# Kernel tuning notes

Measured on AMD Instinct MI355X. Metric: run time of the kernel, lower is better.

The kernel has to match this reference:

```python
import jax, jax.numpy as jnp
import numpy as np

N, E, K, G = 50000, 800000, 3, 64
F_IN, F_HID, F_OUT, N_CLS = 128, 192, 128, 10
LAMBDA_MAX = 2.0  # PyG ChebConv default when lambda_max is None and normalization='sym'


def setup_inputs() -> dict:
    key = jax.random.key(0)
    ks = jax.random.split(key, 12)
    x = jax.random.normal(ks[0], (N, F_IN), dtype=jnp.float32)
    edge_index = jax.random.randint(ks[1], (2, E), 0, N)
    batch = jnp.sort(jax.random.randint(ks[2], (N,), 0, G))

    def mkW(k, fi, fo):
        return jax.random.normal(k, (K, fi, fo), dtype=jnp.float32) / np.float32(np.sqrt(K * fi))

    W1 = mkW(ks[3], F_IN, F_HID)
    b1 = jax.random.normal(ks[4], (F_HID,), dtype=jnp.float32) * 0.01
    W2 = mkW(ks[5], F_HID, F_HID)
    b2 = jax.random.normal(ks[6], (F_HID,), dtype=jnp.float32) * 0.01
    W3 = mkW(ks[7], F_HID, F_OUT)
    b3 = jax.random.normal(ks[8], (F_OUT,), dtype=jnp.float32) * 0.01
    fc_w = jax.random.normal(ks[9], (F_OUT, N_CLS), dtype=jnp.float32) / np.float32(np.sqrt(F_OUT))
    fc_b = jax.random.normal(ks[10], (N_CLS,), dtype=jnp.float32) * 0.01
    return {"x": x, "edge_index": edge_index, "batch": batch,
            "W1": W1, "b1": b1, "W2": W2, "b2": b2, "W3": W3, "b3": b3,
            "fc_w": fc_w, "fc_b": fc_b}


def reference(x, edge_index, batch, W1, b1, W2, b2, W3, b3, fc_w, fc_b):
    row, col = edge_index[0], edge_index[1]
    # symmetric scaled Laplacian: L_hat = (2/lmax) * (I - D^-1/2 A D^-1/2) - I
    deg = jax.ops.segment_sum(jnp.ones((E,), x.dtype), row, num_segments=N)
    dis = jnp.where(deg > 0, jax.lax.rsqrt(jnp.maximum(deg, 1e-12)), 0.0)
    scale = 2.0 / LAMBDA_MAX
    w_edge = (-scale) * dis[row] * dis[col]  # off-diagonal entries of L_hat
    diag_w = scale - 1.0                      # diagonal entries (0 when lmax=2)

    def prop(h):  # h: [N, F] -> L_hat @ h
        return jax.ops.segment_sum(w_edge[:, None] * h[col], row, num_segments=N) + diag_w * h

    def cheb_conv(h, W, b):
        Tx0 = h
        out = Tx0 @ W[0]
        Tx1 = prop(Tx0)
        out = out + Tx1 @ W[1]
        for k in range(2, K):
            Tx2 = 2.0 * prop(Tx1) - Tx0
            out = out + Tx2 @ W[k]
            Tx0, Tx1 = Tx1, Tx2
        return out + b

    h = cheb_conv(x, W1, b1)
    h = cheb_conv(h, W2, b2)
    h = cheb_conv(h, W3, b3)

    # global mean pool over graphs
    sums = jax.ops.segment_sum(h, batch, num_segments=G)
    cnts = jax.ops.segment_sum(jnp.ones((N,), h.dtype), batch, num_segments=G)
    pooled = sums / jnp.maximum(cnts, 1.0)[:, None]  # [G, F_OUT]

    logits = pooled @ fc_w + fc_b
    return jax.nn.log_softmax(logits, axis=1)
```

## Files before the change

### kernel.cpp

```cpp
#include <hip/hip_runtime.h>
#include <math.h>

#define N_NODES 50000
#define N_EDGES 800000
#define N_GRAPHS 64
#define F_INN 128
#define F_HID 192
#define F_OUTT 128
#define N_CLS 10

typedef short short8 __attribute__((ext_vector_type(8)));
typedef float f32x4 __attribute__((ext_vector_type(4)));

static __device__ inline unsigned short f2bf(float f) {
    unsigned int u = __float_as_uint(f);
    unsigned int r = (u + 0x7FFFu + ((u >> 16) & 1u)) >> 16;
    return (unsigned short)r;
}
static __device__ inline float bf2f(unsigned short h) {
    return __uint_as_float(((unsigned int)h) << 16);
}

__global__ void k_deg(const int* __restrict__ row, int* __restrict__ cnt,
                      int* __restrict__ rank) {
    int e = blockIdx.x * 256 + threadIdx.x;
    if (e < N_EDGES) rank[e] = atomicAdd(&cnt[row[e]], 1);
}

__global__ void k_scan1(const int* __restrict__ cnt, int* __restrict__ rp,
                        int* __restrict__ part, float* __restrict__ dis) {
    __shared__ int s[256];
    int base = blockIdx.x * 512;
    int i0 = base + 2 * threadIdx.x;
    int v0 = (i0 < N_NODES) ? cnt[i0] : 0;
    int v1 = (i0 + 1 < N_NODES) ? cnt[i0 + 1] : 0;
    if (i0 < N_NODES) dis[i0] = v0 > 0 ? rsqrtf((float)v0) : 0.f;
    if (i0 + 1 < N_NODES) dis[i0 + 1] = v1 > 0 ? rsqrtf((float)v1) : 0.f;
    int tsum = v0 + v1;
    s[threadIdx.x] = tsum;
    __syncthreads();
    for (int off = 1; off < 256; off <<= 1) {
        int val = (threadIdx.x >= off) ? s[threadIdx.x - off] : 0;
        __syncthreads();
        s[threadIdx.x] += val;
        __syncthreads();
    }
    int excl = s[threadIdx.x] - tsum;
    if (i0 < N_NODES) rp[i0] = excl;
    if (i0 + 1 < N_NODES) rp[i0 + 1] = excl + v0;
    if (threadIdx.x == 255) part[blockIdx.x] = s[255];
}

__global__ void k_scan3(int* __restrict__ rp, const int* __restrict__ part,
                        int nb) {
    __shared__ int s[128];
    int t = threadIdx.x;
    int b = blockIdx.x;
    if (t < 128) s[t] = (t < b && t < nb) ? part[t] : 0;
    __syncthreads();
    for (int off = 64; off > 0; off >>= 1) {
        if (t < off) s[t] += s[t + off];
        __syncthreads();
    }
    int add = s[0];
    int i0 = b * 512 + 2 * t;
    if (i0 < N_NODES) rp[i0] += add;
    if (i0 + 1 < N_NODES) rp[i0 + 1] += add;
    if (b == 0 && t == 0) rp[N_NODES] = N_EDGES;
}

__global__ void k_scatter(const int* __restrict__ row, const int* __restrict__ col,
                          const float* __restrict__ dis, const int* __restrict__ rp,
                          const int* __restrict__ rank, int2* __restrict__ cw) {
    int e = blockIdx.x * 256 + threadIdx.x;
    if (e < N_EDGES) {
        int r = row[e], c = col[e];
        int pos = rp[r] + rank[e];
        int2 v;
        v.x = c;
        v.y = __float_as_int(-dis[r] * dis[c]);
        cw[pos] = v;
    }
}

#define NX (N_NODES * F_INN)
#define NW1 (3 * 128 * 192)
#define NW2 (3 * 192 * 192)
#define NW3 (3 * 192 * 128)
#define NPS (N_GRAPHS * F_OUTT)
__global__ void k_convAll(const float* __restrict__ x, const float* __restrict__ W1,
                          const float* __restrict__ W2, const float* __restrict__ W3,
                          unsigned short* __restrict__ xb,
                          unsigned short* __restrict__ Wt1,
                          unsigned short* __restrict__ Wt2,
                          unsigned short* __restrict__ Wt3,
                          int* __restrict__ cnt, float* __restrict__ psum) {
    int idx = blockIdx.x * 256 + threadIdx.x;
    if (idx < NX) {
        xb[idx] = f2bf(x[idx]);
        return;
    }
    idx -= NX;
    if (idx < NW1) {
        int per = 128 * 192;
        int j = idx / per, r = idx - j * per;
        int k = r / 192, n = r - k * 192;
        float v = (j == 0) ? (W1[idx] - W1[idx + 2 * per])
                           : (j == 2 ? 2.f * W1[idx] : W1[idx]);
        Wt1[j * per + n * 128 + k] = f2bf(v);
        return;
    }
    idx -= NW1;
    if (idx < NW2) {
        int per = 192 * 192;
        int j = idx / per, r = idx - j * per;
        int k = r / 192, n = r - k * 192;
        float v = (j == 0) ? (W2[idx] - W2[idx + 2 * per])
                           : (j == 2 ? 2.f * W2[idx] : W2[idx]);
        Wt2[j * per + n * 192 + k] = f2bf(v);
        return;
    }
    idx -= NW2;
    if (idx < NW3) {
        int per = 192 * 128;
        int j = idx / per, r = idx - j * per;
        int k = r / 128, n = r - k * 128;
        float v = (j == 0) ? (W3[idx] - W3[idx + 2 * per])
                           : (j == 2 ? 2.f * W3[idx] : W3[idx]);
        Wt3[j * per + n * 192 + k] = f2bf(v);
        return;
    }
    idx -= NW3;
    if (idx < N_NODES) {
        cnt[idx] = 0;
        return;
    }
    idx -= N_NODES;
    if (idx < NPS) psum[idx] = 0.f;
}

template <int F>
__global__ void k_spmv(const int* __restrict__ rp, const int2* __restrict__ cw,
                       const unsigned short* __restrict__ h,
                       unsigned short* __restrict__ y) {
    constexpr bool EX = (F > 128);
    constexpr int FU = F / 2;
    int wave = threadIdx.x >> 6;
    int lane = threadIdx.x & 63;
    int r = blockIdx.x * 4 + wave;
    if (r >= N_NODES) return;
    int e0 = __builtin_amdgcn_readfirstlane(rp[r]);
    int e1 = __builtin_amdgcn_readfirstlane(rp[r + 1]);
    const unsigned int* hu = (const unsigned int*)h;
    float a0 = 0.f, a1 = 0.f, a2 = 0.f;
    int e = e0;
    for (; e + 8 <= e1; e += 8) {
        int colv[8];
        float wv[8];
#pragma unroll
        for (int u = 0; u < 8; u++) {
            int2 p = cw[e + u];
            colv[u] = __builtin_amdgcn_readfirstlane(p.x);
            wv[u] = __uint_as_float(__builtin_amdgcn_readfirstlane(p.y));
        }
        unsigned int g[8];
        unsigned short s[8];
#pragma unroll
        for (int u = 0; u < 8; u++) {
            g[u] = hu[colv[u] * FU + lane];
            if constexpr (EX) s[u] = h[colv[u] * F + 128 + lane];
        }
#pragma unroll
        for (int u = 0; u < 8; u++) {
            a0 += wv[u] * bf2f((unsigned short)g[u]);
            a1 += wv[u] * bf2f((unsigned short)(g[u] >> 16));
            if constexpr (EX) a2 += wv[u] * bf2f(s[u]);
        }
    }
    for (; e + 4 <= e1; e += 4) {
        int colv[4];
        float wv[4];
#pragma unroll
        for (int u = 0; u < 4; u++) {
            int2 p = cw[e + u];
            colv[u] = __builtin_amdgcn_readfirstlane(p.x);
            wv[u] = __uint_as_float(__builtin_amdgcn_readfirstlane(p.y));
        }
        unsigned int g[4];
        unsigned short s[4];
#pragma unroll
        for (int u = 0; u < 4; u++) {
            g[u] = hu[colv[u] * FU + lane];
            if constexpr (EX) s[u] = h[colv[u] * F + 128 + lane];
        }
#pragma unroll
        for (int u = 0; u < 4; u++) {
            a0 += wv[u] * bf2f((unsigned short)g[u]);
            a1 += wv[u] * bf2f((unsigned short)(g[u] >> 16));
            if constexpr (EX) a2 += wv[u] * bf2f(s[u]);
        }
    }
    for (; e < e1; e++) {
        int2 p = cw[e];
        int c = __builtin_amdgcn_readfirstlane(p.x);
        float w = __uint_as_float(__builtin_amdgcn_readfirstlane(p.y));
        unsigned int g = hu[c * FU + lane];
        a0 += w * bf2f((unsigned short)g);
        a1 += w * bf2f((unsigned short)(g >> 16));
        if constexpr (EX) a2 += w * bf2f(h[c * F + 128 + lane]);
    }
    ((unsigned int*)y)[r * FU + lane] =
        (unsigned int)f2bf(a0) | ((unsigned int)f2bf(a1) << 16);
    if constexpr (EX) y[r * F + 128 + lane] = f2bf(a2);
}

template <int Fin, int Fout, bool FUSE_POOL>
__global__ __launch_bounds__(256) void k_gemm3(
    const unsigned short* __restrict__ A0, const unsigned short* __restrict__ A1,
    const unsigned short* __restrict__ A2, const unsigned short* __restrict__ Wt,
    const float* __restrict__ bias, unsigned short* __restrict__ C,
    const int* __restrict__ batch, float* __restrict__ psum) {
    constexpr int NF = Fout / 16;
    constexpr int BP = Fout / 64;
    __shared__ unsigned short As[128 * 40];
    __shared__ unsigned short Bs[Fout * 40];
    int t = threadIdx.x;
    int w = t >> 6;
    int lane = t & 63;
    int ml = lane & 15;
    int quad = lane >> 4;
    int mBase = blockIdx.x * 128;
    constexpr int per = Fin * Fout;

    f32x4 acc[2][NF];
#pragma unroll
    for (int i = 0; i < 2; i++)
#pragma unroll
        for (int jn = 0; jn < NF; jn++) acc[i][jn] = (f32x4){0.f, 0.f, 0.f, 0.f};

    int srow = t >> 2;
    int schunk = t & 3;
    constexpr int nChunks = (3 * Fin) >> 5;

    for (int ch = 0; ch < nChunks; ch++) {
        int kg = ch << 5;
        int j = kg / Fin;
        int kk = kg - j * Fin;
        const unsigned short* Aj = (j == 0) ? A0 : (j == 1) ? A1 : A2;
        if (ch > 0) __syncthreads();
#pragma unroll
        for (int pass = 0; pass < 2; pass++) {
            int row = srow + pass * 64;
            int gm = mBase + row;
            uint4 v = {0u, 0u, 0u, 0u};
            if (gm < N_NODES)
                v = *(const uint4*)(Aj + (size_t)gm * Fin + kk + schunk * 8);
            *(uint4*)&As[row * 40 + schunk * 8] = v;
        }
#pragma unroll
        for (int pass = 0; pass < BP; pass++) {
            int row = srow + pass * 64;
            const unsigned short* src =
                Wt + (size_t)j * per + (size_t)row * Fin + kk + schunk * 8;
            *(uint4*)&Bs[row * 40 + schunk * 8] = *(const uint4*)src;
        }
        __syncthreads();

        short8 afr[2];
#pragma unroll
        for (int i = 0; i < 2; i++)
            afr[i] = *(const short8*)&As[(w * 32 + i * 16 + ml) * 40 + quad * 8];
#pragma unroll
        for (int jn = 0; jn < NF; jn++) {
            short8 bfr = *(const short8*)&Bs[(jn * 16 + ml) * 40 + quad * 8];
#pragma unroll
            for (int i = 0; i < 2; i++)
                acc[i][jn] = __builtin_amdgcn_mfma_f32_16x16x32_bf16(
                    afr[i], bfr, acc[i][jn], 0, 0, 0);
        }
    }

    float biasv[NF];
#pragma unroll
    for (int jn = 0; jn < NF; jn++) biasv[jn] = bias[jn * 16 + ml];

    if constexpr (!FUSE_POOL) {
#pragma unroll
        for (int i = 0; i < 2; i++) {
#pragma unroll
            for (int r = 0; r < 4; r++) {
                int m = mBase + w * 32 + i * 16 + quad * 4 + r;
                if (m < N_NODES) {
                    unsigned short* cp = C + (size_t)m * Fout + ml;
#pragma unroll
                    for (int jn = 0; jn < NF; jn++)
                        cp[jn * 16] = f2bf(acc[i][jn][r] + biasv[jn]);
                }
            }
        }
    } else {
        int m0 = mBase + w * 32;
        if (m0 >= N_NODES) return;
        int mlast = m0 + 31;
        if (mlast >= N_NODES) mlast = N_NODES - 1;
        int g0 = batch[m0];
        int g1 = batch[mlast];
        if (g0 == g1) {
#pragma unroll
            for (int jn = 0; jn < NF; jn++) {
                float pv = 0.f;
#pragma unroll
                for (int i = 0; i < 2; i++)
#pragma unroll
                    for (int r = 0; r < 4; r++) {
                        int m = m0 + i * 16 + quad * 4 + r;
                        if (m < N_NODES) pv += acc[i][jn][r] + biasv[jn];
                    }
                pv += __shfl_xor(pv, 16);
                pv += __shfl_xor(pv, 32);
                if (lane < 16) atomicAdd(&psum[g0 * F_OUTT + ml + jn * 16], pv);
            }
        } else {
#pragma unroll
            for (int i = 0; i < 2; i++)
#pragma unroll
                for (int r = 0; r < 4; r++) {
                    int m = m0 + i * 16 + quad * 4 + r;
                    if (m < N_NODES) {
                        int g = batch[m];
#pragma unroll
                        for (int jn = 0; jn < NF; jn++)
                            atomicAdd(&psum[g * F_OUTT + ml + jn * 16],
                                      acc[i][jn][r] + biasv[jn]);
                    }
                }
        }
    }
}

__global__ void k_head(const float* __restrict__ psum, const int* __restrict__ batch,
                       const float* __restrict__ fcw, const float* __restrict__ fcb,
                       float* __restrict__ out) {
    int g = blockIdx.x;
    int c = threadIdx.x;
    __shared__ float sl[N_CLS];
    int a = 0, b = N_NODES;
    while (a < b) { int m = (a + b) >> 1; if (batch[m] < g) a = m + 1; else b = m; }
    int lo = a;
    a = lo; b = N_NODES;
    while (a < b) { int m = (a + b) >> 1; if (batch[m] < g + 1) a = m + 1; else b = m; }
    float inv = 1.f / fmaxf((float)(a - lo), 1.f);
    float l = 0.f;
    if (c < N_CLS) {
        l = fcb[c];
        for (int k = 0; k < F_OUTT; k++)
            l += psum[g * F_OUTT + k] * inv * fcw[k * N_CLS + c];
        sl[c] = l;
    }
    __syncthreads();
    if (c < N_CLS) {
        float m = -1e30f;
        for (int i = 0; i < N_CLS; i++) m = fmaxf(m, sl[i]);
        float s = 0.f;
        for (int i = 0; i < N_CLS; i++) s += expf(sl[i] - m);
        out[g * N_CLS + c] = l - m - logf(s);
    }
}

extern "C" void kernel_launch(void* const* d_in, const int* in_sizes, int n_in,
                              void* d_out, int out_size, void* d_ws, size_t ws_size,
                              hipStream_t stream) {
    const float* x = (const float*)d_in[0];
    const int* ei = (const int*)d_in[1];
    const int* batch = (const int*)d_in[2];
    const float* W1 = (const float*)d_in[3];
    const float* b1 = (const float*)d_in[4];
    const float* W2 = (const float*)d_in[5];
    const float* b2 = (const float*)d_in[6];
    const float* W3 = (const float*)d_in[7];
    const float* b3 = (const float*)d_in[8];
    const float* fcw = (const float*)d_in[9];
    const float* fcb = (const float*)d_in[10];
    float* out = (float*)d_out;
    const int* row = ei;
    const int* col = ei + N_EDGES;

    char* p = (char*)d_ws;
    auto carve = [&](size_t bytes) {
        char* q = p;
        p += (bytes + 255) & ~(size_t)255;
        return q;
    };
    int* cnt = (int*)carve(N_NODES * 4);
    int* rank = (int*)carve((size_t)N_EDGES * 4);
    float* dis = (float*)carve(N_NODES * 4);
    int* rp = (int*)carve((N_NODES + 1) * 4);
    int* part = (int*)carve(128 * 4);
    int2* cw = (int2*)carve((size_t)N_EDGES * 8);
    unsigned short* xb = (unsigned short*)carve((size_t)N_NODES * F_INN * 2);
    size_t hbytes = (size_t)N_NODES * 192 * 2;
    unsigned short* bufA = (unsigned short*)carve(hbytes);
    unsigned short* bufB = (unsigned short*)carve(hbytes);
    unsigned short* bufC = (unsigned short*)carve(hbytes);
    unsigned short* bufD = (unsigned short*)carve(hbytes);
    unsigned short* Wt1 = (unsigned short*)carve(NW1 * 2);
    unsigned short* Wt2 = (unsigned short*)carve(NW2 * 2);
    unsigned short* Wt3 = (unsigned short*)carve(NW3 * 2);
    float* psum = (float*)carve(NPS * 4);

    {
        int tot = NX + NW1 + NW2 + NW3 + N_NODES + NPS;
        k_convAll<<<(tot + 255) / 256, 256, 0, stream>>>(x, W1, W2, W3, xb, Wt1, Wt2,
                                                         Wt3, cnt, psum);
    }

    k_deg<<<(N_EDGES + 255) / 256, 256, 0, stream>>>(row, cnt, rank);
    int nb = (N_NODES + 511) / 512;
    k_scan1<<<nb, 256, 0, stream>>>(cnt, rp, part, dis);
    k_scan3<<<nb, 256, 0, stream>>>(rp, part, nb);
    k_scatter<<<(N_EDGES + 255) / 256, 256, 0, stream>>>(row, col, dis, rp, rank, cw);

    const int spmvGrid = (N_NODES + 3) / 4;
    const int gemmGrid = (N_NODES + 127) / 128;

    k_spmv<128><<<spmvGrid, 256, 0, stream>>>(rp, cw, xb, bufB);
    k_spmv<128><<<spmvGrid, 256, 0, stream>>>(rp, cw, bufB, bufC);
    k_gemm3<128, 192, false><<<gemmGrid, 256, 0, stream>>>(xb, bufB, bufC, Wt1, b1,
                                                           bufA, batch, psum);
    k_spmv<192><<<spmvGrid, 256, 0, stream>>>(rp, cw, bufA, bufB);
    k_spmv<192><<<spmvGrid, 256, 0, stream>>>(rp, cw, bufB, bufC);
    k_gemm3<192, 192, false><<<gemmGrid, 256, 0, stream>>>(bufA, bufB, bufC, Wt2, b2,
                                                           bufD, batch, psum);
    k_spmv<192><<<spmvGrid, 256, 0, stream>>>(rp, cw, bufD, bufB);
    k_spmv<192><<<spmvGrid, 256, 0, stream>>>(rp, cw, bufB, bufC);
    k_gemm3<192, 128, true><<<gemmGrid, 256, 0, stream>>>(bufD, bufB, bufC, Wt3, b3,
                                                          nullptr, batch, psum);

    k_head<<<N_GRAPHS, 64, 0, stream>>>(psum, batch, fcw, fcb, out);
}
```

Baseline: 456.3 us.

## Pool before final Chebyshev GEMM and compress edge list to 16-bit columns

Uses linearity of mean pooling to drop the third layer's big GEMM. Pooled sums of h, L·h and L²·h are accumulated into psum, and the 192→128 projection is done per graph in the head kernel. The edge array shrinks from (int col, float weight) pairs to 16-bit column indices, and the weight is recomputed in the SpMV from dis values, which cuts edge-stream bandwidth. Risks are atomic contention on psum in the last two SpMVs, extra gathers of dis[col], and the 16-bit index only holding while N fits in 65536.

```diff
diff --git a/kernel.cpp b/kernel.cpp
--- a/kernel.cpp
+++ b/kernel.cpp
@@ -19,6 +19,9 @@
 }
 static __device__ inline float bf2f(unsigned short h) {
     return __uint_as_float(((unsigned int)h) << 16);
+}
+static __device__ inline float rfl_f(float v) {
+    return __uint_as_float(__builtin_amdgcn_readfirstlane(__float_as_uint(v)));
 }
 
 __global__ void k_deg(const int* __restrict__ row, int* __restrict__ cnt,
@@ -70,16 +73,12 @@
 }
 
 __global__ void k_scatter(const int* __restrict__ row, const int* __restrict__ col,
-                          const float* __restrict__ dis, const int* __restrict__ rp,
-                          const int* __restrict__ rank, int2* __restrict__ cw) {
+                          const int* __restrict__ rp, const int* __restrict__ rank,
+                          unsigned short* __restrict__ cols16) {
     int e = blockIdx.x * 256 + threadIdx.x;
     if (e < N_EDGES) {
-        int r = row[e], c = col[e];
-        int pos = rp[r] + rank[e];
-        int2 v;
-        v.x = c;
-        v.y = __float_as_int(-dis[r] * dis[c]);
-        cw[pos] = v;
+        int r = row[e];
+        cols16[rp[r] + rank[e]] = (unsigned short)col[e];
     }
 }
 
@@ -87,7 +86,7 @@
 #define NW1 (3 * 128 * 192)
 #define NW2 (3 * 192 * 192)
 #define NW3 (3 * 192 * 128)
-#define NPS (N_GRAPHS * F_OUTT)
+#define NPS (3 * N_GRAPHS * F_HID)
 __global__ void k_convAll(const float* __restrict__ x, const float* __restrict__ W1,
                           const float* __restrict__ W2, const float* __restrict__ W3,
                           unsigned short* __restrict__ xb,
@@ -139,82 +138,109 @@
     if (idx < NPS) psum[idx] = 0.f;
 }
 
-template <int F>
-__global__ void k_spmv(const int* __restrict__ rp, const int2* __restrict__ cw,
+template <int F, int POOL>
+__global__ void k_spmv(const int* __restrict__ rp,
+                       const unsigned short* __restrict__ cols,
+                       const float* __restrict__ dis,
                        const unsigned short* __restrict__ h,
-                       unsigned short* __restrict__ y) {
+                       unsigned short* __restrict__ y,
+                       const int* __restrict__ batch, float* __restrict__ psum) {
     constexpr bool EX = (F > 128);
     constexpr int FU = F / 2;
+    __shared__ float ps[POOL ? 192 : 1];
+    __shared__ int gs[4];
     int wave = threadIdx.x >> 6;
     int lane = threadIdx.x & 63;
     int r = blockIdx.x * 4 + wave;
-    if (r >= N_NODES) return;
     int e0 = __builtin_amdgcn_readfirstlane(rp[r]);
     int e1 = __builtin_amdgcn_readfirstlane(rp[r + 1]);
+    float ndisr = -rfl_f(dis[r]);
     const unsigned int* hu = (const unsigned int*)h;
     float a0 = 0.f, a1 = 0.f, a2 = 0.f;
     int e = e0;
     for (; e + 8 <= e1; e += 8) {
         int colv[8];
-        float wv[8];
-#pragma unroll
-        for (int u = 0; u < 8; u++) {
-            int2 p = cw[e + u];
-            colv[u] = __builtin_amdgcn_readfirstlane(p.x);
-            wv[u] = __uint_as_float(__builtin_amdgcn_readfirstlane(p.y));
-        }
+#pragma unroll
+        for (int u = 0; u < 8; u++)
+            colv[u] = __builtin_amdgcn_readfirstlane((int)cols[e + u]);
         unsigned int g[8];
         unsigned short s[8];
+        float dv[8];
 #pragma unroll
         for (int u = 0; u < 8; u++) {
             g[u] = hu[colv[u] * FU + lane];
             if constexpr (EX) s[u] = h[colv[u] * F + 128 + lane];
+            dv[u] = rfl_f(dis[colv[u]]);
         }
 #pragma unroll
         for (int u = 0; u < 8; u++) {
-            a0 += wv[u] * bf2f((unsigned short)g[u]);
-            a1 += wv[u] * bf2f((unsigned short)(g[u] >> 16));
-            if constexpr (EX) a2 += wv[u] * bf2f(s[u]);
+            float w = ndisr * dv[u];
+            a0 += w * bf2f((unsigned short)g[u]);
+            a1 += w * bf2f((unsigned short)(g[u] >> 16));
+            if constexpr (EX) a2 += w * bf2f(s[u]);
         }
     }
     for (; e + 4 <= e1; e += 4) {
         int colv[4];
-        float wv[4];
-#pragma unroll
-        for (int u = 0; u < 4; u++) {
-            int2 p = cw[e + u];
-            colv[u] = __builtin_amdgcn_readfirstlane(p.x);
-            wv[u] = __uint_as_float(__builtin_amdgcn_readfirstlane(p.y));
-        }
+#pragma unroll
+        for (int u = 0; u < 4; u++)
+            colv[u] = __builtin_amdgcn_readfirstlane((int)cols[e + u]);
         unsigned int g[4];
         unsigned short s[4];
+        float dv[4];
 #pragma unroll
         for (int u = 0; u < 4; u++) {
             g[u] = hu[colv[u] * FU + lane];
             if constexpr (EX) s[u] = h[colv[u] * F + 128 + lane];
+            dv[u] = rfl_f(dis[colv[u]]);
         }
 #pragma unroll
         for (int u = 0; u < 4; u++) {
-            a0 += wv[u] * bf2f((unsigned short)g[u]);
-            a1 += wv[u] * bf2f((unsigned short)(g[u] >> 16));
-            if constexpr (EX) a2 += wv[u] * bf2f(s[u]);
+            float w = ndisr * dv[u];
+            a0 += w * bf2f((unsigned short)g[u]);
+            a1 += w * bf2f((unsigned short)(g[u] >> 16));
+            if constexpr (EX) a2 += w * bf2f(s[u]);
         }
     }
     for (; e < e1; e++) {
-        int2 p = cw[e];
-        int c = __builtin_amdgcn_readfirstlane(p.x);
-        float w = __uint_as_float(__builtin_amdgcn_readfirstlane(p.y));
+        int c = __builtin_amdgcn_readfirstlane((int)cols[e]);
+        float w = ndisr * rfl_f(dis[c]);
         unsigned int g = hu[c * FU + lane];
         a0 += w * bf2f((unsigned short)g);
         a1 += w * bf2f((unsigned short)(g >> 16));
         if constexpr (EX) a2 += w * bf2f(h[c * F + 128 + lane]);
     }
-    ((unsigned int*)y)[r * FU + lane] =
-        (unsigned int)f2bf(a0) | ((unsigned int)f2bf(a1) << 16);
-    if constexpr (EX) y[r * F + 128 + lane] = f2bf(a2);
-}
-
-template <int Fin, int Fout, bool FUSE_POOL>
+    if constexpr (POOL != 1) {
+        ((unsigned int*)y)[r * FU + lane] =
+            (unsigned int)f2bf(a0) | ((unsigned int)f2bf(a1) << 16);
+        if constexpr (EX) y[r * F + 128 + lane] = f2bf(a2);
+    }
+    if constexpr (POOL != 0) {
+        int t = threadIdx.x;
+        if (t < 4) gs[t] = batch[blockIdx.x * 4 + t];
+        if (t >= 64) ps[t - 64] = 0.f;
+        __syncthreads();
+        int g0 = gs[0], g3 = gs[3];
+        if (g0 == g3) {
+            atomicAdd(&ps[2 * lane], a0);
+            atomicAdd(&ps[2 * lane + 1], a1);
+            atomicAdd(&ps[128 + lane], a2);
+            __syncthreads();
+            if (wave == 0) {
+                atomicAdd(&psum[g0 * 192 + 2 * lane], ps[2 * lane]);
+                atomicAdd(&psum[g0 * 192 + 2 * lane + 1], ps[2 * lane + 1]);
+                atomicAdd(&psum[g0 * 192 + 128 + lane], ps[128 + lane]);
+            }
+        } else {
+            int gg = gs[wave];
+            atomicAdd(&psum[gg * 192 + 2 * lane], a0);
+            atomicAdd(&psum[gg * 192 + 2 * lane + 1], a1);
+            atomicAdd(&psum[gg * 192 + 128 + lane], a2);
+        }
+    }
+}
+
+template <int Fin, int Fout, bool POOL>
 __global__ __launch_bounds__(256) void k_gemm3(
     const unsigned short* __restrict__ A0, const unsigned short* __restrict__ A1,
     const unsigned short* __restrict__ A2, const unsigned short* __restrict__ Wt,
@@ -284,21 +310,20 @@
 #pragma unroll
     for (int jn = 0; jn < NF; jn++) biasv[jn] = bias[jn * 16 + ml];
 
-    if constexpr (!FUSE_POOL) {
-#pragma unroll
-        for (int i = 0; i < 2; i++) {
-#pragma unroll
-            for (int r = 0; r < 4; r++) {
-                int m = mBase + w * 32 + i * 16 + quad * 4 + r;
-                if (m < N_NODES) {
-                    unsigned short* cp = C + (size_t)m * Fout + ml;
-#pragma unroll
-                    for (int jn = 0; jn < NF; jn++)
-                        cp[jn * 16] = f2bf(acc[i][jn][r] + biasv[jn]);
-                }
+#pragma unroll
+    for (int i = 0; i < 2; i++) {
+#pragma unroll
+        for (int r = 0; r < 4; r++) {
+            int m = mBase + w * 32 + i * 16 + quad * 4 + r;
+            if (m < N_NODES) {
+                unsigned short* cp = C + (size_t)m * Fout + ml;
+#pragma unroll
+                for (int jn = 0; jn < NF; jn++)
+                    cp[jn * 16] = f2bf(acc[i][jn][r] + biasv[jn]);
             }
         }
-    } else {
+    }
+    if constexpr (POOL) {
         int m0 = mBase + w * 32;
         if (m0 >= N_NODES) return;
         int mlast = m0 + 31;
@@ -318,7 +343,7 @@
                     }
                 pv += __shfl_xor(pv, 16);
                 pv += __shfl_xor(pv, 32);
-                if (lane < 16) atomicAdd(&psum[g0 * F_OUTT + ml + jn * 16], pv);
+                if (lane < 16) atomicAdd(&psum[g0 * Fout + ml + jn * 16], pv);
             }
         } else {
 #pragma unroll
@@ -330,7 +355,7 @@
                         int g = batch[m];
 #pragma unroll
                         for (int jn = 0; jn < NF; jn++)
-                            atomicAdd(&psum[g * F_OUTT + ml + jn * 16],
+                            atomicAdd(&psum[g * Fout + ml + jn * 16],
                                       acc[i][jn][r] + biasv[jn]);
                     }
                 }
@@ -338,32 +363,56 @@
     }
 }
 
-__global__ void k_head(const float* __restrict__ psum, const int* __restrict__ batch,
-                       const float* __restrict__ fcw, const float* __restrict__ fcb,
-                       float* __restrict__ out) {
+__global__ __launch_bounds__(128) void k_head2(
+    const float* __restrict__ psum,
+    const unsigned short* __restrict__ Wt3, const float* __restrict__ b3,
+    const int* __restrict__ batch, const float* __restrict__ fcw,
+    const float* __restrict__ fcb, float* __restrict__ out) {
     int g = blockIdx.x;
-    int c = threadIdx.x;
+    int t = threadIdx.x;
+    __shared__ float ps[3 * 192];
+    __shared__ float m3[F_OUTT];
     __shared__ float sl[N_CLS];
+    for (int i = t; i < 192; i += 128) {
+        ps[i] = psum[g * 192 + i];
+        ps[192 + i] = psum[N_GRAPHS * 192 + g * 192 + i];
+        ps[384 + i] = psum[2 * N_GRAPHS * 192 + g * 192 + i];
+    }
+    __syncthreads();
     int a = 0, b = N_NODES;
     while (a < b) { int m = (a + b) >> 1; if (batch[m] < g) a = m + 1; else b = m; }
     int lo = a;
     a = lo; b = N_NODES;
     while (a < b) { int m = (a + b) >> 1; if (batch[m] < g + 1) a = m + 1; else b = m; }
     float inv = 1.f / fmaxf((float)(a - lo), 1.f);
-    float l = 0.f;
-    if (c < N_CLS) {
-        l = fcb[c];
-        for (int k = 0; k < F_OUTT; k++)
-            l += psum[g * F_OUTT + k] * inv * fcw[k * N_CLS + c];
-        sl[c] = l;
-    }
+    constexpr int per = 192 * F_OUTT;
+    float accv = 0.f;
+    const unsigned short* wp = Wt3 + (size_t)t * 192;
+#pragma unroll 4
+    for (int k = 0; k < 192; k += 8) {
+        short8 v0 = *(const short8*)(wp + k);
+        short8 v1 = *(const short8*)(wp + per + k);
+        short8 v2 = *(const short8*)(wp + 2 * per + k);
+#pragma unroll
+        for (int j = 0; j < 8; j++)
+            accv += ps[k + j] * bf2f((unsigned short)v0[j]) +
+                    ps[192 + k + j] * bf2f((unsigned short)v1[j]) +
+                    ps[384 + k + j] * bf2f((unsigned short)v2[j]);
+    }
+    m3[t] = accv * inv + b3[t];
     __syncthreads();
-    if (c < N_CLS) {
-        float m = -1e30f;
-        for (int i = 0; i < N_CLS; i++) m = fmaxf(m, sl[i]);
+    if (t < N_CLS) {
+        float l = fcb[t];
+        for (int n = 0; n < F_OUTT; n++) l += m3[n] * fcw[n * N_CLS + t];
+        sl[t] = l;
+    }
+    __syncthreads();
+    if (t < N_CLS) {
+        float mx = -1e30f;
+        for (int i = 0; i < N_CLS; i++) mx = fmaxf(mx, sl[i]);
         float s = 0.f;
-        for (int i = 0; i < N_CLS; i++) s += expf(sl[i] - m);
-        out[g * N_CLS + c] = l - m - logf(s);
+        for (int i = 0; i < N_CLS; i++) s += expf(sl[i] - mx);
+        out[g * N_CLS + t] = sl[t] - mx - logf(s);
     }
 }
 
@@ -396,7 +445,7 @@
     float* dis = (float*)carve(N_NODES * 4);
     int* rp = (int*)carve((N_NODES + 1) * 4);
     int* part = (int*)carve(128 * 4);
-    int2* cw = (int2*)carve((size_t)N_EDGES * 8);
+    unsigned short* cols16 = (unsigned short*)carve((size_t)N_EDGES * 2);
     unsigned short* xb = (unsigned short*)carve((size_t)N_NODES * F_INN * 2);
     size_t hbytes = (size_t)N_NODES * 192 * 2;
     unsigned short* bufA = (unsigned short*)carve(hbytes);
@@ -407,6 +456,9 @@
     unsigned short* Wt2 = (unsigned short*)carve(NW2 * 2);
     unsigned short* Wt3 = (unsigned short*)carve(NW3 * 2);
     float* psum = (float*)carve(NPS * 4);
+    float* psumX = psum;
+    float* psumG1 = psum + N_GRAPHS * 192;
+    float* psumG2 = psum + 2 * N_GRAPHS * 192;
 
     {
         int tot = NX + NW1 + NW2 + NW3 + N_NODES + NPS;
@@ -418,23 +470,27 @@
     int nb = (N_NODES + 511) / 512;
     k_scan1<<<nb, 256, 0, stream>>>(cnt, rp, part, dis);
     k_scan3<<<nb, 256, 0, stream>>>(rp, part, nb);
-    k_scatter<<<(N_EDGES + 255) / 256, 256, 0, stream>>>(row, col, dis, rp, rank, cw);
-
-    const int spmvGrid = (N_NODES + 3) / 4;
+    k_scatter<<<(N_EDGES + 255) / 256, 256, 0, stream>>>(row, col, rp, rank, cols16);
+
+    const int spmvGrid = N_NODES / 4;
     const int gemmGrid = (N_NODES + 127) / 128;
 
-    k_spmv<128><<<spmvGrid, 256, 0, stream>>>(rp, cw, xb, bufB);
-    k_spmv<128><<<spmvGrid, 256, 0, stream>>>(rp, cw, bufB, bufC);
+    k_spmv<128, 0><<<spmvGrid, 256, 0, stream>>>(rp, cols16, dis, xb, bufB, nullptr,
+                                                 nullptr);
+    k_spmv<128, 0><<<spmvGrid, 256, 0, stream>>>(rp, cols16, dis, bufB, bufC, nullptr,
+                                                 nullptr);
     k_gemm3<128, 192, false><<<gemmGrid, 256, 0, stream>>>(xb, bufB, bufC, Wt1, b1,
-                                                           bufA, batch, psum);
-    k_spmv<192><<<spmvGrid, 256, 0, stream>>>(rp, cw, bufA, bufB);
-    k_spmv<192><<<spmvGrid, 256, 0, stream>>>(rp, cw, bufB, bufC);
-    k_gemm3<192, 192, false><<<gemmGrid, 256, 0, stream>>>(bufA, bufB, bufC, Wt2, b2,
-                                                           bufD, batch, psum);
-    k_spmv<192><<<spmvGrid, 256, 0, stream>>>(rp, cw, bufD, bufB);
-    k_spmv<192><<<spmvGrid, 256, 0, stream>>>(rp, cw, bufB, bufC);
-    k_gemm3<192, 128, true><<<gemmGrid, 256, 0, stream>>>(bufD, bufB, bufC, Wt3, b3,
-                                                          nullptr, batch, psum);
-
-    k_head<<<N_GRAPHS, 64, 0, stream>>>(psum, batch, fcw, fcb, out);
-}
+                                                           bufA, batch, nullptr);
+    k_spmv<192, 0><<<spmvGrid, 256, 0, stream>>>(rp, cols16, dis, bufA, bufB, nullptr,
+                                                 nullptr);
+    k_spmv<192, 0><<<spmvGrid, 256, 0, stream>>>(rp, cols16, dis, bufB, bufC, nullptr,
+                                                 nullptr);
+    k_gemm3<192, 192, true><<<gemmGrid, 256, 0, stream>>>(bufA, bufB, bufC, Wt2, b2,
+                                                          bufD, batch, psumX);
+    k_spmv<192, 2><<<spmvGrid, 256, 0, stream>>>(rp, cols16, dis, bufD, bufB, batch,
+                                                 psumG1);
+    k_spmv<192, 1><<<spmvGrid, 256, 0, stream>>>(rp, cols16, dis, bufB, nullptr, batch,
+                                                 psumG2);
+
+    k_head2<<<N_GRAPHS, 128, 0, stream>>>(psum, Wt3, b3, batch, fcw, fcb, out);
+}
```

New measurement: 565.0 us. 23.8% more time.
